# Kernel optimization log

Measured on AMD Instinct MI355X. Metric: run time of the kernel, lower is better.

## Reference

```python
import jax, jax.numpy as jnp
import numpy as np

B, S, D, E, K, FF = 4, 2048, 1024, 8, 2, 4096  # batch, seq, d_model, experts, top-k, 4*d_model


def setup_inputs() -> dict:
    key = jax.random.key(0)
    k0, k1, k2, k3 = jax.random.split(key, 4)
    scale = 0.02
    return {
        "x": jax.random.normal(k0, (B, S, D), jnp.float32),
        "gate_w": jax.random.normal(k1, (D, E), jnp.float32) * scale,
        "w1": jax.random.normal(k2, (E, D, FF), jnp.float32) * scale,
        "b1": jnp.zeros((E, FF), jnp.float32),
        "w2": jax.random.normal(k3, (E, FF, D), jnp.float32) * scale,
        "b2": jnp.zeros((E, D), jnp.float32),
    }


def reference(x, gate_w, w1, b1, w2, b2):
    # Gating: top-k logits, softmax over the selected k (matches torch.topk + softmax)
    logits = jnp.einsum("bsd,de->bse", x, gate_w)  # [B,S,E]
    vals, idxs = jax.lax.top_k(logits, K)           # [B,S,K]
    w = jax.nn.softmax(vals, axis=-1)               # [B,S,K]
    n_exp = gate_w.shape[-1]
    # Per-token combine weight for each expert (0 if not selected)
    combine = jnp.sum(jax.nn.one_hot(idxs, n_exp, dtype=x.dtype) * w[..., None], axis=-2)  # [B,S,E]

    out = jnp.zeros_like(x)
    for e in range(n_exp):  # fixed small loop over experts
        h = jax.nn.silu(jnp.einsum("bsd,df->bsf", x, w1[e]) + b1[e])  # dropout = identity (eval)
        y = jnp.einsum("bsf,fd->bsd", h, w2[e]) + b2[e]
        out = out + combine[..., e:e + 1] * y
    return out
```

## Files before the change

kernel.cpp:

```cpp
#include <hip/hip_runtime.h>
#include <math.h>

#define Tt 8192
#define Dd 1024
#define Ee 8
#define FFf 4096
#define SLOTS (Tt*2)

typedef unsigned short u16;
typedef unsigned int u32;
typedef __attribute__((ext_vector_type(8))) __bf16 bf16x8;
typedef __attribute__((ext_vector_type(4))) float f32x4;

__device__ __forceinline__ u16 f2bf(float f) {
  union { float f; u32 u; } v; v.f = f;
  u32 u = v.u;
  return (u16)((u + 0x7FFFu + ((u >> 16) & 1u)) >> 16);
}
__device__ __forceinline__ float bf2f(u16 h) {
  union { u32 u; float f; } v; v.u = ((u32)h) << 16; return v.f;
}
__device__ __forceinline__ void gl2lds16(const u16* g, u16* l) {
  __builtin_amdgcn_global_load_lds((const __attribute__((address_space(1))) void*)g,
                                   (__attribute__((address_space(3))) void*)l, 16, 0, 0);
}

__global__ void gate_topk_kernel(const float* __restrict__ x,
                                 const float* __restrict__ gw,
                                 int* __restrict__ counts,
                                 int* __restrict__ tok_e,
                                 float* __restrict__ tok_w) {
  int wave = (int)((blockIdx.x * blockDim.x + threadIdx.x) >> 6);
  int lane = threadIdx.x & 63;
  if (wave >= Tt) return;
  const float* xrow = x + (size_t)wave * Dd;
  float p[Ee];
#pragma unroll
  for (int e = 0; e < Ee; e++) p[e] = 0.f;
  int d0 = lane * 16;
#pragma unroll
  for (int i = 0; i < 16; i++) {
    float xv = xrow[d0 + i];
    const float* g = gw + (size_t)(d0 + i) * Ee;
#pragma unroll
    for (int e = 0; e < Ee; e++) p[e] += xv * g[e];
  }
#pragma unroll
  for (int e = 0; e < Ee; e++) {
    for (int off = 32; off > 0; off >>= 1) p[e] += __shfl_xor(p[e], off, 64);
  }
  if (lane == 0) {
    int e0 = 0; float v0 = p[0];
#pragma unroll
    for (int e = 1; e < Ee; e++) if (p[e] > v0) { v0 = p[e]; e0 = e; }
    int e1 = -1; float v1 = -INFINITY;
#pragma unroll
    for (int e = 0; e < Ee; e++) if (e != e0 && p[e] > v1) { v1 = p[e]; e1 = e; }
    float w0 = 1.f / (1.f + expf(v1 - v0));
    float w1 = 1.f - w0;
    tok_e[wave * 2 + 0] = e0; tok_e[wave * 2 + 1] = e1;
    tok_w[wave * 2 + 0] = w0; tok_w[wave * 2 + 1] = w1;
    atomicAdd(&counts[e0], 1);
    atomicAdd(&counts[e1], 1);
  }
}

__global__ void xb_convert_kernel(const float* __restrict__ x, u16* __restrict__ xb) {
  int i = blockIdx.x * blockDim.x + threadIdx.x;
  const float* s = x + (size_t)i * 8;
  f32x4 v0 = *(const f32x4*)(s);
  f32x4 v1 = *(const f32x4*)(s + 4);
  uint4 o;
  o.x = (u32)f2bf(v0[0]) | ((u32)f2bf(v0[1]) << 16);
  o.y = (u32)f2bf(v0[2]) | ((u32)f2bf(v0[3]) << 16);
  o.z = (u32)f2bf(v1[0]) | ((u32)f2bf(v1[1]) << 16);
  o.w = (u32)f2bf(v1[2]) | ((u32)f2bf(v1[3]) << 16);
  *(uint4*)(xb + (size_t)i * 8) = o;
}

__global__ __launch_bounds__(256) void wconv_kernel(const float* __restrict__ src,
                                                    u16* __restrict__ dst, int R, int C) {
  __shared__ float t[64][65];
  int e = blockIdx.z;
  size_t ebase = (size_t)e * R * C;
  int r0 = blockIdx.y * 64, c0 = blockIdx.x * 64;
  int tid = threadIdx.x;
  int row = tid >> 2, q = tid & 3;
  const float* sp = src + ebase + (size_t)(r0 + row) * C + c0 + q * 16;
  f32x4 v0 = *(const f32x4*)(sp);
  f32x4 v1 = *(const f32x4*)(sp + 4);
  f32x4 v2 = *(const f32x4*)(sp + 8);
  f32x4 v3 = *(const f32x4*)(sp + 12);
#pragma unroll
  for (int k = 0; k < 4; k++) t[row][q * 16 + k] = v0[k];
#pragma unroll
  for (int k = 0; k < 4; k++) t[row][q * 16 + 4 + k] = v1[k];
#pragma unroll
  for (int k = 0; k < 4; k++) t[row][q * 16 + 8 + k] = v2[k];
#pragma unroll
  for (int k = 0; k < 4; k++) t[row][q * 16 + 12 + k] = v3[k];
  __syncthreads();
  float c[16];
#pragma unroll
  for (int k = 0; k < 16; k++) c[k] = t[q * 16 + k][row];
  uint4 d0, d1;
  d0.x = (u32)f2bf(c[0]) | ((u32)f2bf(c[1]) << 16);
  d0.y = (u32)f2bf(c[2]) | ((u32)f2bf(c[3]) << 16);
  d0.z = (u32)f2bf(c[4]) | ((u32)f2bf(c[5]) << 16);
  d0.w = (u32)f2bf(c[6]) | ((u32)f2bf(c[7]) << 16);
  d1.x = (u32)f2bf(c[8]) | ((u32)f2bf(c[9]) << 16);
  d1.y = (u32)f2bf(c[10]) | ((u32)f2bf(c[11]) << 16);
  d1.z = (u32)f2bf(c[12]) | ((u32)f2bf(c[13]) << 16);
  d1.w = (u32)f2bf(c[14]) | ((u32)f2bf(c[15]) << 16);
  u16* dp = dst + ebase + (size_t)(c0 + row) * R + r0 + q * 16;
  *(uint4*)dp = d0;
  *(uint4*)(dp + 8) = d1;
}

__global__ void scan_kernel(const int* __restrict__ counts,
                            int* __restrict__ offsets, int* __restrict__ cursors) {
  if (threadIdx.x == 0 && blockIdx.x == 0) {
    int acc = 0;
    for (int e = 0; e < Ee; e++) { offsets[e] = acc; cursors[e] = acc; acc += counts[e]; }
  }
}

__global__ void scatter_kernel(const int* __restrict__ tok_e, const float* __restrict__ tok_w,
                               int* __restrict__ cursors,
                               int* __restrict__ slot_token, float* __restrict__ slot_w,
                               int* __restrict__ tok_slot) {
  int t = blockIdx.x * blockDim.x + threadIdx.x;
  if (t >= Tt) return;
#pragma unroll
  for (int k = 0; k < 2; k++) {
    int e = tok_e[t * 2 + k];
    int pos = atomicAdd(&cursors[e], 1);
    slot_token[pos] = t;
    slot_w[pos] = tok_w[t * 2 + k];
    tok_slot[t * 2 + k] = pos;
  }
}

#define MFMA16(H)                                                                 \
  do {                                                                            \
    acc[H][0][0] = __builtin_amdgcn_mfma_f32_16x16x32_bf16(a0, b0, acc[H][0][0], 0, 0, 0); \
    acc[H][0][1] = __builtin_amdgcn_mfma_f32_16x16x32_bf16(a0, b1, acc[H][0][1], 0, 0, 0); \
    acc[H][0][2] = __builtin_amdgcn_mfma_f32_16x16x32_bf16(a0, b2, acc[H][0][2], 0, 0, 0); \
    acc[H][0][3] = __builtin_amdgcn_mfma_f32_16x16x32_bf16(a0, b3, acc[H][0][3], 0, 0, 0); \
    acc[H][1][0] = __builtin_amdgcn_mfma_f32_16x16x32_bf16(a1, b0, acc[H][1][0], 0, 0, 0); \
    acc[H][1][1] = __builtin_amdgcn_mfma_f32_16x16x32_bf16(a1, b1, acc[H][1][1], 0, 0, 0); \
    acc[H][1][2] = __builtin_amdgcn_mfma_f32_16x16x32_bf16(a1, b2, acc[H][1][2], 0, 0, 0); \
    acc[H][1][3] = __builtin_amdgcn_mfma_f32_16x16x32_bf16(a1, b3, acc[H][1][3], 0, 0, 0); \
    acc[H][2][0] = __builtin_amdgcn_mfma_f32_16x16x32_bf16(a2, b0, acc[H][2][0], 0, 0, 0); \
    acc[H][2][1] = __builtin_amdgcn_mfma_f32_16x16x32_bf16(a2, b1, acc[H][2][1], 0, 0, 0); \
    acc[H][2][2] = __builtin_amdgcn_mfma_f32_16x16x32_bf16(a2, b2, acc[H][2][2], 0, 0, 0); \
    acc[H][2][3] = __builtin_amdgcn_mfma_f32_16x16x32_bf16(a2, b3, acc[H][2][3], 0, 0, 0); \
    acc[H][3][0] = __builtin_amdgcn_mfma_f32_16x16x32_bf16(a3, b0, acc[H][3][0], 0, 0, 0); \
    acc[H][3][1] = __builtin_amdgcn_mfma_f32_16x16x32_bf16(a3, b1, acc[H][3][1], 0, 0, 0); \
    acc[H][3][2] = __builtin_amdgcn_mfma_f32_16x16x32_bf16(a3, b2, acc[H][3][2], 0, 0, 0); \
    acc[H][3][3] = __builtin_amdgcn_mfma_f32_16x16x32_bf16(a3, b3, acc[H][3][3], 0, 0, 0); \
  } while (0)

template<int KDIM, int NDIM, int EPI, int GATHER>
__global__ __launch_bounds__(512, 2) void moe_gemm_big(
    const u16* __restrict__ A, const u16* __restrict__ BT,
    const float* __restrict__ bias,
    const int* __restrict__ offsets, const int* __restrict__ counts,
    const int* __restrict__ slot_token, const float* __restrict__ slot_w,
    u16* __restrict__ O16, float* __restrict__ Of) {
  constexpr int NT = KDIM / 64;
  int e = blockIdx.z;
  int cnt = counts[e];
  int rb = blockIdx.y;
  if (rb * 256 >= cnt) return;
  int off = offsets[e];
  int n0 = blockIdx.x * 256;

  __shared__ u16 S[65536];

  int tid = threadIdx.x;
  int lane = tid & 63, wave = tid >> 6;
  int wr = wave >> 2, wc = wave & 3;
  int lr = lane & 15, g = lane >> 4;

  const u16* BTe = BT + (size_t)e * NDIM * KDIM;

  const u16* aSrc[2][2];
  const u16* bSrc[2][2];
  int amax = off + cnt - 1;
#pragma unroll
  for (int h = 0; h < 2; h++)
#pragma unroll
    for (int s = 0; s < 2; s++) {
      int c = tid + s * 512;
      int lc = c ^ (((c >> 5) & 1) << 1);
      int ks = lc >> 9, rl = (lc >> 2) & 127, seg = lc & 3;
      int slotRow = off + rb * 256 + h * 128 + rl;
      if (slotRow > amax) slotRow = amax;
      int arow = GATHER ? slot_token[slotRow] : slotRow;
      aSrc[h][s] = A + (size_t)arow * KDIM + ks * 32 + seg * 8;
    }
#pragma unroll
  for (int ks = 0; ks < 2; ks++)
#pragma unroll
    for (int s = 0; s < 2; s++) {
      int c = tid + s * 512;
      int lc = c ^ (((c >> 5) & 1) << 1);
      int row = lc >> 2, seg = lc & 3;
      bSrc[ks][s] = BTe + (size_t)(n0 + row) * KDIM + ks * 32 + seg * 8;
    }

  auto stA = [&](int u, int h) {
    u16* d = &S[(u & 1) * 16384 + h * 8192 + wave * 512];
    gl2lds16(aSrc[h][0] + (size_t)u * 64, d);
    gl2lds16(aSrc[h][1] + (size_t)u * 64, d + 4096);
  };
  auto stB = [&](int u, int ks) {
    u16* d = &S[32768 + (u & 1) * 16384 + ks * 8192 + wave * 512];
    gl2lds16(bSrc[ks][0] + (size_t)u * 64, d);
    gl2lds16(bSrc[ks][1] + (size_t)u * 64, d + 4096);
  };
  auto rdA = [&](int dbuf, int hm, int ks, int i) -> bf16x8 {
    int rl = wr * 64 + i * 16 + lr;
    int logb = ks * 8192 + rl * 64 + g * 16;
    int phys = logb ^ (((rl >> 3) & 1) << 5);
    return *reinterpret_cast<const bf16x8*>(&S[dbuf * 16384 + hm * 8192 + (phys >> 1)]);
  };
  auto rdB = [&](int dbuf, int ks, int j) -> bf16x8 {
    int row = wc * 64 + j * 16 + lr;
    int logb = row * 64 + g * 16;
    int phys = logb ^ (((row >> 3) & 1) << 5);
    return *reinterpret_cast<const bf16x8*>(&S[32768 + dbuf * 16384 + ks * 8192 + (phys >> 1)]);
  };

  f32x4 acc[2][4][4];
#pragma unroll
  for (int h = 0; h < 2; h++)
#pragma unroll
    for (int i = 0; i < 4; i++)
#pragma unroll
      for (int j = 0; j < 4; j++) acc[h][i][j] = (f32x4)(0.0f);

  stB(0, 0); stA(0, 0); stA(0, 1); stB(0, 1);
  stB(1, 0); stA(1, 0);
  asm volatile("s_waitcnt vmcnt(4)" ::: "memory");
  __builtin_amdgcn_s_barrier();

  bf16x8 b0, b1, b2, b3;
  for (int t = 0; t < NT; ++t) {
    int dbuf = t & 1;
    {
      bf16x8 a0 = rdA(dbuf, 0, 0, 0), a1 = rdA(dbuf, 0, 0, 1),
             a2 = rdA(dbuf, 0, 0, 2), a3 = rdA(dbuf, 0, 0, 3);
      b0 = rdB(dbuf, 0, 0); b1 = rdB(dbuf, 0, 1); b2 = rdB(dbuf, 0, 2); b3 = rdB(dbuf, 0, 3);
      if (t + 1 < NT) stA(t + 1, 1);
      __builtin_amdgcn_s_barrier();
      asm volatile("s_waitcnt lgkmcnt(0)" ::: "memory");
      __builtin_amdgcn_sched_barrier(0);
      __builtin_amdgcn_s_setprio(1);
      MFMA16(0);
      __builtin_amdgcn_s_setprio(0);
      __builtin_amdgcn_s_barrier();
    }
    {
      bf16x8 a0 = rdA(dbuf, 1, 0, 0), a1 = rdA(dbuf, 1, 0, 1),
             a2 = rdA(dbuf, 1, 0, 2), a3 = rdA(dbuf, 1, 0, 3);
      if (t + 1 < NT) {
        stB(t + 1, 1);
        asm volatile("s_waitcnt vmcnt(6)" ::: "memory");
      }
      __builtin_amdgcn_s_barrier();
      asm volatile("s_waitcnt lgkmcnt(0)" ::: "memory");
      __builtin_amdgcn_sched_barrier(0);
      __builtin_amdgcn_s_setprio(1);
      MFMA16(1);
      __builtin_amdgcn_s_setprio(0);
      __builtin_amdgcn_s_barrier();
    }
    {
      bf16x8 a0 = rdA(dbuf, 0, 1, 0), a1 = rdA(dbuf, 0, 1, 1),
             a2 = rdA(dbuf, 0, 1, 2), a3 = rdA(dbuf, 0, 1, 3);
      b0 = rdB(dbuf, 1, 0); b1 = rdB(dbuf, 1, 1); b2 = rdB(dbuf, 1, 2); b3 = rdB(dbuf, 1, 3);
      if (t + 2 < NT) stB(t + 2, 0);
      __builtin_amdgcn_s_barrier();
      asm volatile("s_waitcnt lgkmcnt(0)" ::: "memory");
      __builtin_amdgcn_sched_barrier(0);
      __builtin_amdgcn_s_setprio(1);
      MFMA16(0);
      __builtin_amdgcn_s_setprio(0);
      __builtin_amdgcn_s_barrier();
    }
    {
      bf16x8 a0 = rdA(dbuf, 1, 1, 0), a1 = rdA(dbuf, 1, 1, 1),
             a2 = rdA(dbuf, 1, 1, 2), a3 = rdA(dbuf, 1, 1, 3);
      if (t + 2 < NT) {
        stA(t + 2, 0);
        asm volatile("s_waitcnt vmcnt(6)" ::: "memory");
      } else if (t + 1 < NT) {
        asm volatile("s_waitcnt vmcnt(0)" ::: "memory");
      }
      __builtin_amdgcn_s_barrier();
      asm volatile("s_waitcnt lgkmcnt(0)" ::: "memory");
      __builtin_amdgcn_sched_barrier(0);
      __builtin_amdgcn_s_setprio(1);
      MFMA16(1);
      __builtin_amdgcn_s_setprio(0);
      __builtin_amdgcn_s_barrier();
    }
  }

  int rlim = cnt - rb * 256;
#pragma unroll
  for (int hm = 0; hm < 2; hm++)
#pragma unroll
    for (int i = 0; i < 4; i++)
#pragma unroll
      for (int q = 0; q < 4; q++) {
        int m = hm * 128 + wr * 64 + i * 16 + g * 4 + q;
        if (m < rlim) {
          int slot = off + rb * 256 + m;
#pragma unroll
          for (int j = 0; j < 4; j++) {
            int n = n0 + wc * 64 + j * 16 + lr;
            float v = acc[hm][i][j][q] + bias[e * NDIM + n];
            if (EPI == 0) {
              float sv = v / (1.f + expf(-v));
              O16[(size_t)slot * NDIM + n] = f2bf(sv);
            } else if (EPI == 1) {
              O16[(size_t)slot * NDIM + n] = f2bf(v * slot_w[slot]);
            } else {
              atomicAdd(Of + (size_t)slot_token[slot] * NDIM + n, v * slot_w[slot]);
            }
          }
        }
      }
}

__global__ void combine_kernel(const u16* __restrict__ y, const int* __restrict__ tok_slot,
                               float* __restrict__ out) {
  int gid = blockIdx.x * blockDim.x + threadIdx.x;
  int t = gid >> 7;
  int seg = gid & 127;
  int s0 = tok_slot[t * 2 + 0], s1 = tok_slot[t * 2 + 1];
  uint4 a = *(const uint4*)(y + (size_t)s0 * Dd + seg * 8);
  uint4 b = *(const uint4*)(y + (size_t)s1 * Dd + seg * 8);
  f32x4 o0, o1;
  o0[0] = bf2f((u16)a.x) + bf2f((u16)b.x);
  o0[1] = bf2f((u16)(a.x >> 16)) + bf2f((u16)(b.x >> 16));
  o0[2] = bf2f((u16)a.y) + bf2f((u16)b.y);
  o0[3] = bf2f((u16)(a.y >> 16)) + bf2f((u16)(b.y >> 16));
  o1[0] = bf2f((u16)a.z) + bf2f((u16)b.z);
  o1[1] = bf2f((u16)(a.z >> 16)) + bf2f((u16)(b.z >> 16));
  o1[2] = bf2f((u16)a.w) + bf2f((u16)b.w);
  o1[3] = bf2f((u16)(a.w >> 16)) + bf2f((u16)(b.w >> 16));
  float* op = out + (size_t)t * Dd + seg * 8;
  *(f32x4*)op = o0;
  *(f32x4*)(op + 4) = o1;
}

extern "C" void kernel_launch(void* const* d_in, const int* in_sizes, int n_in,
                              void* d_out, int out_size, void* d_ws, size_t ws_size,
                              hipStream_t stream) {
  const float* x  = (const float*)d_in[0];
  const float* gw = (const float*)d_in[1];
  const float* w1 = (const float*)d_in[2];
  const float* b1 = (const float*)d_in[3];
  const float* w2 = (const float*)d_in[4];
  const float* b2 = (const float*)d_in[5];
  float* out = (float*)d_out;

  char* ws = (char*)d_ws;
  size_t off_counts = 0;
  size_t off_offsets = 256;
  size_t off_cursors = 512;
  size_t off_tok_e = 1024;
  size_t off_tok_w     = off_tok_e + (size_t)Tt * 2 * 4;
  size_t off_tok_slot  = off_tok_w + (size_t)Tt * 2 * 4;
  size_t off_slot_token= off_tok_slot + (size_t)Tt * 2 * 4;
  size_t off_slot_w    = off_slot_token + (size_t)SLOTS * 4;
  size_t off_xb        = off_slot_w + (size_t)SLOTS * 4;
  size_t off_h         = off_xb + (size_t)Tt * Dd * 2;
  size_t off_wT        = off_h + (size_t)SLOTS * FFf * 2;
  size_t off_y         = off_wT + (size_t)Ee * Dd * FFf * 2;
  size_t need_atomic   = off_y;
  size_t need_full     = off_y + (size_t)SLOTS * Dd * 2;
  if (ws_size < need_atomic) return;
  int use_combine = (ws_size >= need_full) ? 1 : 0;

  int* counts     = (int*)(ws + off_counts);
  int* offsets    = (int*)(ws + off_offsets);
  int* cursors    = (int*)(ws + off_cursors);
  int* tok_e      = (int*)(ws + off_tok_e);
  float* tok_w    = (float*)(ws + off_tok_w);
  int* tok_slot   = (int*)(ws + off_tok_slot);
  int* slot_token = (int*)(ws + off_slot_token);
  float* slot_w   = (float*)(ws + off_slot_w);
  u16* xb         = (u16*)(ws + off_xb);
  u16* h          = (u16*)(ws + off_h);
  u16* wT         = (u16*)(ws + off_wT);
  u16* y          = (u16*)(ws + off_y);

  hipMemsetAsync(ws, 0, 1024, stream);

  gate_topk_kernel<<<Tt / 4, 256, 0, stream>>>(x, gw, counts, tok_e, tok_w);
  xb_convert_kernel<<<(Tt * Dd / 8) / 256, 256, 0, stream>>>(x, xb);
  scan_kernel<<<1, 64, 0, stream>>>(counts, offsets, cursors);
  scatter_kernel<<<Tt / 256, 256, 0, stream>>>(tok_e, tok_w, cursors, slot_token, slot_w, tok_slot);

  {
    dim3 gc(FFf / 64, Dd / 64, Ee);
    wconv_kernel<<<gc, 256, 0, stream>>>(w1, wT, Dd, FFf);
  }
  {
    dim3 g1(FFf / 256, Tt / 256, Ee);
    moe_gemm_big<Dd, FFf, 0, 1><<<g1, 512, 0, stream>>>(xb, wT, b1, offsets, counts,
                                                        slot_token, slot_w, h, nullptr);
  }
  {
    dim3 gc(Dd / 64, FFf / 64, Ee);
    wconv_kernel<<<gc, 256, 0, stream>>>(w2, wT, FFf, Dd);
  }
  if (use_combine) {
    dim3 g2(Dd / 256, Tt / 256, Ee);
    moe_gemm_big<FFf, Dd, 1, 0><<<g2, 512, 0, stream>>>(h, wT, b2, offsets, counts,
                                                        slot_token, slot_w, y, nullptr);
    combine_kernel<<<(Tt * 128) / 256, 256, 0, stream>>>(y, tok_slot, out);
  } else {
    hipMemsetAsync(d_out, 0, (size_t)out_size * sizeof(float), stream);
    dim3 g2(Dd / 256, Tt / 256, Ee);
    moe_gemm_big<FFf, Dd, 2, 0><<<g2, 512, 0, stream>>>(h, wT, b2, offsets, counts,
                                                        slot_token, slot_w, nullptr, out);
  }
}
```

Baseline: 793.2 us.

## Shrink MoE GEMM row tile to 128 and fuse bf16 cast into gating

The grouped expert GEMM now uses a 128x256 output tile instead of 256x256. The k-step pipeline drops from four MFMA phases to two, shared memory shrinks, and the grid gets more blocks in the row dimension. This is meant to cut padding waste from ragged per-expert token counts and to spread work across more CUs, at the cost of less B-tile reuse per block. Separately, the fp32-to-bf16 conversion of x moves into the gating kernel, which already reads x, so the standalone conversion kernel and its extra pass over x are removed.

```diff
diff --git a/kernel.cpp b/kernel.cpp
--- a/kernel.cpp
+++ b/kernel.cpp
@@ -29,7 +29,8 @@
                                  const float* __restrict__ gw,
                                  int* __restrict__ counts,
                                  int* __restrict__ tok_e,
-                                 float* __restrict__ tok_w) {
+                                 float* __restrict__ tok_w,
+                                 u16* __restrict__ xb) {
   int wave = (int)((blockIdx.x * blockDim.x + threadIdx.x) >> 6);
   int lane = threadIdx.x & 63;
   if (wave >= Tt) return;
@@ -38,12 +39,27 @@
 #pragma unroll
   for (int e = 0; e < Ee; e++) p[e] = 0.f;
   int d0 = lane * 16;
+  float xv[16];
 #pragma unroll
   for (int i = 0; i < 16; i++) {
-    float xv = xrow[d0 + i];
+    xv[i] = xrow[d0 + i];
     const float* g = gw + (size_t)(d0 + i) * Ee;
 #pragma unroll
-    for (int e = 0; e < Ee; e++) p[e] += xv * g[e];
+    for (int e = 0; e < Ee; e++) p[e] += xv[i] * g[e];
+  }
+  {
+    uint4 o0, o1;
+    o0.x = (u32)f2bf(xv[0]) | ((u32)f2bf(xv[1]) << 16);
+    o0.y = (u32)f2bf(xv[2]) | ((u32)f2bf(xv[3]) << 16);
+    o0.z = (u32)f2bf(xv[4]) | ((u32)f2bf(xv[5]) << 16);
+    o0.w = (u32)f2bf(xv[6]) | ((u32)f2bf(xv[7]) << 16);
+    o1.x = (u32)f2bf(xv[8]) | ((u32)f2bf(xv[9]) << 16);
+    o1.y = (u32)f2bf(xv[10]) | ((u32)f2bf(xv[11]) << 16);
+    o1.z = (u32)f2bf(xv[12]) | ((u32)f2bf(xv[13]) << 16);
+    o1.w = (u32)f2bf(xv[14]) | ((u32)f2bf(xv[15]) << 16);
+    u16* dp = xb + (size_t)wave * Dd + d0;
+    *(uint4*)dp = o0;
+    *(uint4*)(dp + 8) = o1;
   }
 #pragma unroll
   for (int e = 0; e < Ee; e++) {
@@ -63,19 +79,6 @@
     atomicAdd(&counts[e0], 1);
     atomicAdd(&counts[e1], 1);
   }
-}
-
-__global__ void xb_convert_kernel(const float* __restrict__ x, u16* __restrict__ xb) {
-  int i = blockIdx.x * blockDim.x + threadIdx.x;
-  const float* s = x + (size_t)i * 8;
-  f32x4 v0 = *(const f32x4*)(s);
-  f32x4 v1 = *(const f32x4*)(s + 4);
-  uint4 o;
-  o.x = (u32)f2bf(v0[0]) | ((u32)f2bf(v0[1]) << 16);
-  o.y = (u32)f2bf(v0[2]) | ((u32)f2bf(v0[3]) << 16);
-  o.z = (u32)f2bf(v1[0]) | ((u32)f2bf(v1[1]) << 16);
-  o.w = (u32)f2bf(v1[2]) | ((u32)f2bf(v1[3]) << 16);
-  *(uint4*)(xb + (size_t)i * 8) = o;
 }
 
 __global__ __launch_bounds__(256) void wconv_kernel(const float* __restrict__ src,
@@ -141,28 +144,28 @@
   }
 }
 
-#define MFMA16(H)                                                                 \
+#define MFMA16R                                                                   \
   do {                                                                            \
-    acc[H][0][0] = __builtin_amdgcn_mfma_f32_16x16x32_bf16(a0, b0, acc[H][0][0], 0, 0, 0); \
-    acc[H][0][1] = __builtin_amdgcn_mfma_f32_16x16x32_bf16(a0, b1, acc[H][0][1], 0, 0, 0); \
-    acc[H][0][2] = __builtin_amdgcn_mfma_f32_16x16x32_bf16(a0, b2, acc[H][0][2], 0, 0, 0); \
-    acc[H][0][3] = __builtin_amdgcn_mfma_f32_16x16x32_bf16(a0, b3, acc[H][0][3], 0, 0, 0); \
-    acc[H][1][0] = __builtin_amdgcn_mfma_f32_16x16x32_bf16(a1, b0, acc[H][1][0], 0, 0, 0); \
-    acc[H][1][1] = __builtin_amdgcn_mfma_f32_16x16x32_bf16(a1, b1, acc[H][1][1], 0, 0, 0); \
-    acc[H][1][2] = __builtin_amdgcn_mfma_f32_16x16x32_bf16(a1, b2, acc[H][1][2], 0, 0, 0); \
-    acc[H][1][3] = __builtin_amdgcn_mfma_f32_16x16x32_bf16(a1, b3, acc[H][1][3], 0, 0, 0); \
-    acc[H][2][0] = __builtin_amdgcn_mfma_f32_16x16x32_bf16(a2, b0, acc[H][2][0], 0, 0, 0); \
-    acc[H][2][1] = __builtin_amdgcn_mfma_f32_16x16x32_bf16(a2, b1, acc[H][2][1], 0, 0, 0); \
-    acc[H][2][2] = __builtin_amdgcn_mfma_f32_16x16x32_bf16(a2, b2, acc[H][2][2], 0, 0, 0); \
-    acc[H][2][3] = __builtin_amdgcn_mfma_f32_16x16x32_bf16(a2, b3, acc[H][2][3], 0, 0, 0); \
-    acc[H][3][0] = __builtin_amdgcn_mfma_f32_16x16x32_bf16(a3, b0, acc[H][3][0], 0, 0, 0); \
-    acc[H][3][1] = __builtin_amdgcn_mfma_f32_16x16x32_bf16(a3, b1, acc[H][3][1], 0, 0, 0); \
-    acc[H][3][2] = __builtin_amdgcn_mfma_f32_16x16x32_bf16(a3, b2, acc[H][3][2], 0, 0, 0); \
-    acc[H][3][3] = __builtin_amdgcn_mfma_f32_16x16x32_bf16(a3, b3, acc[H][3][3], 0, 0, 0); \
+    acc[0][0] = __builtin_amdgcn_mfma_f32_16x16x32_bf16(a0, b0, acc[0][0], 0, 0, 0); \
+    acc[0][1] = __builtin_amdgcn_mfma_f32_16x16x32_bf16(a0, b1, acc[0][1], 0, 0, 0); \
+    acc[0][2] = __builtin_amdgcn_mfma_f32_16x16x32_bf16(a0, b2, acc[0][2], 0, 0, 0); \
+    acc[0][3] = __builtin_amdgcn_mfma_f32_16x16x32_bf16(a0, b3, acc[0][3], 0, 0, 0); \
+    acc[1][0] = __builtin_amdgcn_mfma_f32_16x16x32_bf16(a1, b0, acc[1][0], 0, 0, 0); \
+    acc[1][1] = __builtin_amdgcn_mfma_f32_16x16x32_bf16(a1, b1, acc[1][1], 0, 0, 0); \
+    acc[1][2] = __builtin_amdgcn_mfma_f32_16x16x32_bf16(a1, b2, acc[1][2], 0, 0, 0); \
+    acc[1][3] = __builtin_amdgcn_mfma_f32_16x16x32_bf16(a1, b3, acc[1][3], 0, 0, 0); \
+    acc[2][0] = __builtin_amdgcn_mfma_f32_16x16x32_bf16(a2, b0, acc[2][0], 0, 0, 0); \
+    acc[2][1] = __builtin_amdgcn_mfma_f32_16x16x32_bf16(a2, b1, acc[2][1], 0, 0, 0); \
+    acc[2][2] = __builtin_amdgcn_mfma_f32_16x16x32_bf16(a2, b2, acc[2][2], 0, 0, 0); \
+    acc[2][3] = __builtin_amdgcn_mfma_f32_16x16x32_bf16(a2, b3, acc[2][3], 0, 0, 0); \
+    acc[3][0] = __builtin_amdgcn_mfma_f32_16x16x32_bf16(a3, b0, acc[3][0], 0, 0, 0); \
+    acc[3][1] = __builtin_amdgcn_mfma_f32_16x16x32_bf16(a3, b1, acc[3][1], 0, 0, 0); \
+    acc[3][2] = __builtin_amdgcn_mfma_f32_16x16x32_bf16(a3, b2, acc[3][2], 0, 0, 0); \
+    acc[3][3] = __builtin_amdgcn_mfma_f32_16x16x32_bf16(a3, b3, acc[3][3], 0, 0, 0); \
   } while (0)
 
 template<int KDIM, int NDIM, int EPI, int GATHER>
-__global__ __launch_bounds__(512, 2) void moe_gemm_big(
+__global__ __launch_bounds__(512, 2) void moe_gemm_r(
     const u16* __restrict__ A, const u16* __restrict__ BT,
     const float* __restrict__ bias,
     const int* __restrict__ offsets, const int* __restrict__ counts,
@@ -172,11 +175,11 @@
   int e = blockIdx.z;
   int cnt = counts[e];
   int rb = blockIdx.y;
-  if (rb * 256 >= cnt) return;
+  if (rb * 128 >= cnt) return;
   int off = offsets[e];
   int n0 = blockIdx.x * 256;
 
-  __shared__ u16 S[65536];
+  __shared__ u16 S[49152];
 
   int tid = threadIdx.x;
   int lane = tid & 63, wave = tid >> 6;
@@ -185,117 +188,85 @@
 
   const u16* BTe = BT + (size_t)e * NDIM * KDIM;
 
-  const u16* aSrc[2][2];
-  const u16* bSrc[2][2];
+  const u16* aSrc[2];
+  const u16* bSrc[4];
   int amax = off + cnt - 1;
 #pragma unroll
-  for (int h = 0; h < 2; h++)
-#pragma unroll
-    for (int s = 0; s < 2; s++) {
-      int c = tid + s * 512;
-      int lc = c ^ (((c >> 5) & 1) << 1);
-      int ks = lc >> 9, rl = (lc >> 2) & 127, seg = lc & 3;
-      int slotRow = off + rb * 256 + h * 128 + rl;
-      if (slotRow > amax) slotRow = amax;
-      int arow = GATHER ? slot_token[slotRow] : slotRow;
-      aSrc[h][s] = A + (size_t)arow * KDIM + ks * 32 + seg * 8;
-    }
-#pragma unroll
-  for (int ks = 0; ks < 2; ks++)
-#pragma unroll
-    for (int s = 0; s < 2; s++) {
-      int c = tid + s * 512;
-      int lc = c ^ (((c >> 5) & 1) << 1);
-      int row = lc >> 2, seg = lc & 3;
-      bSrc[ks][s] = BTe + (size_t)(n0 + row) * KDIM + ks * 32 + seg * 8;
-    }
-
-  auto stA = [&](int u, int h) {
-    u16* d = &S[(u & 1) * 16384 + h * 8192 + wave * 512];
-    gl2lds16(aSrc[h][0] + (size_t)u * 64, d);
-    gl2lds16(aSrc[h][1] + (size_t)u * 64, d + 4096);
+  for (int s = 0; s < 2; s++) {
+    int c = tid + s * 512;
+    int lc = c ^ (((c >> 5) & 1) << 1);
+    int rl = (lc >> 2) & 127, seg = lc & 3;
+    int slotRow = off + rb * 128 + rl;
+    if (slotRow > amax) slotRow = amax;
+    int arow = GATHER ? slot_token[slotRow] : slotRow;
+    aSrc[s] = A + (size_t)arow * KDIM + s * 32 + seg * 8;
+  }
+#pragma unroll
+  for (int s = 0; s < 4; s++) {
+    int c = tid + s * 512;
+    int lc = c ^ (((c >> 5) & 1) << 1);
+    int row = (lc >> 2) & 255, seg = lc & 3;
+    int ks = s >> 1;
+    bSrc[s] = BTe + (size_t)(n0 + row) * KDIM + ks * 32 + seg * 8;
+  }
+
+  auto stA = [&](int u, int ks) {
+    gl2lds16(aSrc[ks] + (size_t)u * 64, &S[(u & 1) * 8192 + ks * 4096 + wave * 512]);
   };
   auto stB = [&](int u, int ks) {
-    u16* d = &S[32768 + (u & 1) * 16384 + ks * 8192 + wave * 512];
-    gl2lds16(bSrc[ks][0] + (size_t)u * 64, d);
-    gl2lds16(bSrc[ks][1] + (size_t)u * 64, d + 4096);
+    u16* base = &S[16384 + (u & 1) * 16384 + ks * 8192 + wave * 512];
+    gl2lds16(bSrc[ks * 2] + (size_t)u * 64, base);
+    gl2lds16(bSrc[ks * 2 + 1] + (size_t)u * 64, base + 4096);
   };
-  auto rdA = [&](int dbuf, int hm, int ks, int i) -> bf16x8 {
+  auto rdA = [&](int dbuf, int ks, int i) -> bf16x8 {
     int rl = wr * 64 + i * 16 + lr;
-    int logb = ks * 8192 + rl * 64 + g * 16;
+    int logb = rl * 64 + g * 16;
     int phys = logb ^ (((rl >> 3) & 1) << 5);
-    return *reinterpret_cast<const bf16x8*>(&S[dbuf * 16384 + hm * 8192 + (phys >> 1)]);
+    return *reinterpret_cast<const bf16x8*>(&S[dbuf * 8192 + ks * 4096 + (phys >> 1)]);
   };
   auto rdB = [&](int dbuf, int ks, int j) -> bf16x8 {
     int row = wc * 64 + j * 16 + lr;
     int logb = row * 64 + g * 16;
     int phys = logb ^ (((row >> 3) & 1) << 5);
-    return *reinterpret_cast<const bf16x8*>(&S[32768 + dbuf * 16384 + ks * 8192 + (phys >> 1)]);
+    return *reinterpret_cast<const bf16x8*>(&S[16384 + dbuf * 16384 + ks * 8192 + (phys >> 1)]);
   };
 
-  f32x4 acc[2][4][4];
-#pragma unroll
-  for (int h = 0; h < 2; h++)
-#pragma unroll
-    for (int i = 0; i < 4; i++)
-#pragma unroll
-      for (int j = 0; j < 4; j++) acc[h][i][j] = (f32x4)(0.0f);
-
-  stB(0, 0); stA(0, 0); stA(0, 1); stB(0, 1);
+  f32x4 acc[4][4];
+#pragma unroll
+  for (int i = 0; i < 4; i++)
+#pragma unroll
+    for (int j = 0; j < 4; j++) acc[i][j] = (f32x4)(0.0f);
+
+  stB(0, 0); stA(0, 0);
+  stB(0, 1); stA(0, 1);
   stB(1, 0); stA(1, 0);
-  asm volatile("s_waitcnt vmcnt(4)" ::: "memory");
+  asm volatile("s_waitcnt vmcnt(3)" ::: "memory");
   __builtin_amdgcn_s_barrier();
 
-  bf16x8 b0, b1, b2, b3;
   for (int t = 0; t < NT; ++t) {
     int dbuf = t & 1;
     {
-      bf16x8 a0 = rdA(dbuf, 0, 0, 0), a1 = rdA(dbuf, 0, 0, 1),
-             a2 = rdA(dbuf, 0, 0, 2), a3 = rdA(dbuf, 0, 0, 3);
-      b0 = rdB(dbuf, 0, 0); b1 = rdB(dbuf, 0, 1); b2 = rdB(dbuf, 0, 2); b3 = rdB(dbuf, 0, 3);
-      if (t + 1 < NT) stA(t + 1, 1);
+      bf16x8 a0 = rdA(dbuf, 0, 0), a1 = rdA(dbuf, 0, 1),
+             a2 = rdA(dbuf, 0, 2), a3 = rdA(dbuf, 0, 3);
+      bf16x8 b0 = rdB(dbuf, 0, 0), b1 = rdB(dbuf, 0, 1),
+             b2 = rdB(dbuf, 0, 2), b3 = rdB(dbuf, 0, 3);
+      if (t + 1 < NT) { stB(t + 1, 1); stA(t + 1, 1); }
       __builtin_amdgcn_s_barrier();
       asm volatile("s_waitcnt lgkmcnt(0)" ::: "memory");
       __builtin_amdgcn_sched_barrier(0);
       __builtin_amdgcn_s_setprio(1);
-      MFMA16(0);
+      MFMA16R;
       __builtin_amdgcn_s_setprio(0);
       __builtin_amdgcn_s_barrier();
     }
     {
-      bf16x8 a0 = rdA(dbuf, 1, 0, 0), a1 = rdA(dbuf, 1, 0, 1),
-             a2 = rdA(dbuf, 1, 0, 2), a3 = rdA(dbuf, 1, 0, 3);
-      if (t + 1 < NT) {
-        stB(t + 1, 1);
-        asm volatile("s_waitcnt vmcnt(6)" ::: "memory");
-      }
-      __builtin_amdgcn_s_barrier();
-      asm volatile("s_waitcnt lgkmcnt(0)" ::: "memory");
-      __builtin_amdgcn_sched_barrier(0);
-      __builtin_amdgcn_s_setprio(1);
-      MFMA16(1);
-      __builtin_amdgcn_s_setprio(0);
-      __builtin_amdgcn_s_barrier();
-    }
-    {
-      bf16x8 a0 = rdA(dbuf, 0, 1, 0), a1 = rdA(dbuf, 0, 1, 1),
-             a2 = rdA(dbuf, 0, 1, 2), a3 = rdA(dbuf, 0, 1, 3);
-      b0 = rdB(dbuf, 1, 0); b1 = rdB(dbuf, 1, 1); b2 = rdB(dbuf, 1, 2); b3 = rdB(dbuf, 1, 3);
-      if (t + 2 < NT) stB(t + 2, 0);
-      __builtin_amdgcn_s_barrier();
-      asm volatile("s_waitcnt lgkmcnt(0)" ::: "memory");
-      __builtin_amdgcn_sched_barrier(0);
-      __builtin_amdgcn_s_setprio(1);
-      MFMA16(0);
-      __builtin_amdgcn_s_setprio(0);
-      __builtin_amdgcn_s_barrier();
-    }
-    {
-      bf16x8 a0 = rdA(dbuf, 1, 1, 0), a1 = rdA(dbuf, 1, 1, 1),
-             a2 = rdA(dbuf, 1, 1, 2), a3 = rdA(dbuf, 1, 1, 3);
+      bf16x8 a0 = rdA(dbuf, 1, 0), a1 = rdA(dbuf, 1, 1),
+             a2 = rdA(dbuf, 1, 2), a3 = rdA(dbuf, 1, 3);
+      bf16x8 b0 = rdB(dbuf, 1, 0), b1 = rdB(dbuf, 1, 1),
+             b2 = rdB(dbuf, 1, 2), b3 = rdB(dbuf, 1, 3);
       if (t + 2 < NT) {
-        stA(t + 2, 0);
-        asm volatile("s_waitcnt vmcnt(6)" ::: "memory");
+        stB(t + 2, 0); stA(t + 2, 0);
+        asm volatile("s_waitcnt vmcnt(3)" ::: "memory");
       } else if (t + 1 < NT) {
         asm volatile("s_waitcnt vmcnt(0)" ::: "memory");
       }
@@ -303,37 +274,35 @@
       asm volatile("s_waitcnt lgkmcnt(0)" ::: "memory");
       __builtin_amdgcn_sched_barrier(0);
       __builtin_amdgcn_s_setprio(1);
-      MFMA16(1);
+      MFMA16R;
       __builtin_amdgcn_s_setprio(0);
       __builtin_amdgcn_s_barrier();
     }
   }
 
-  int rlim = cnt - rb * 256;
-#pragma unroll
-  for (int hm = 0; hm < 2; hm++)
-#pragma unroll
-    for (int i = 0; i < 4; i++)
-#pragma unroll
-      for (int q = 0; q < 4; q++) {
-        int m = hm * 128 + wr * 64 + i * 16 + g * 4 + q;
-        if (m < rlim) {
-          int slot = off + rb * 256 + m;
-#pragma unroll
-          for (int j = 0; j < 4; j++) {
-            int n = n0 + wc * 64 + j * 16 + lr;
-            float v = acc[hm][i][j][q] + bias[e * NDIM + n];
-            if (EPI == 0) {
-              float sv = v / (1.f + expf(-v));
-              O16[(size_t)slot * NDIM + n] = f2bf(sv);
-            } else if (EPI == 1) {
-              O16[(size_t)slot * NDIM + n] = f2bf(v * slot_w[slot]);
-            } else {
-              atomicAdd(Of + (size_t)slot_token[slot] * NDIM + n, v * slot_w[slot]);
-            }
+  int rlim = cnt - rb * 128;
+#pragma unroll
+  for (int i = 0; i < 4; i++)
+#pragma unroll
+    for (int q = 0; q < 4; q++) {
+      int m = wr * 64 + i * 16 + g * 4 + q;
+      if (m < rlim) {
+        int slot = off + rb * 128 + m;
+#pragma unroll
+        for (int j = 0; j < 4; j++) {
+          int n = n0 + wc * 64 + j * 16 + lr;
+          float v = acc[i][j][q] + bias[e * NDIM + n];
+          if (EPI == 0) {
+            float sv = v / (1.f + expf(-v));
+            O16[(size_t)slot * NDIM + n] = f2bf(sv);
+          } else if (EPI == 1) {
+            O16[(size_t)slot * NDIM + n] = f2bf(v * slot_w[slot]);
+          } else {
+            atomicAdd(Of + (size_t)slot_token[slot] * NDIM + n, v * slot_w[slot]);
           }
         }
       }
+    }
 }
 
 __global__ void combine_kernel(const u16* __restrict__ y, const int* __restrict__ tok_slot,
@@ -402,8 +371,7 @@
 
   hipMemsetAsync(ws, 0, 1024, stream);
 
-  gate_topk_kernel<<<Tt / 4, 256, 0, stream>>>(x, gw, counts, tok_e, tok_w);
-  xb_convert_kernel<<<(Tt * Dd / 8) / 256, 256, 0, stream>>>(x, xb);
+  gate_topk_kernel<<<Tt / 4, 256, 0, stream>>>(x, gw, counts, tok_e, tok_w, xb);
   scan_kernel<<<1, 64, 0, stream>>>(counts, offsets, cursors);
   scatter_kernel<<<Tt / 256, 256, 0, stream>>>(tok_e, tok_w, cursors, slot_token, slot_w, tok_slot);
 
@@ -412,23 +380,23 @@
     wconv_kernel<<<gc, 256, 0, stream>>>(w1, wT, Dd, FFf);
   }
   {
-    dim3 g1(FFf / 256, Tt / 256, Ee);
-    moe_gemm_big<Dd, FFf, 0, 1><<<g1, 512, 0, stream>>>(xb, wT, b1, offsets, counts,
-                                                        slot_token, slot_w, h, nullptr);
+    dim3 g1(FFf / 256, 64, Ee);
+    moe_gemm_r<Dd, FFf, 0, 1><<<g1, 512, 0, stream>>>(xb, wT, b1, offsets, counts,
+                                                      slot_token, slot_w, h, nullptr);
   }
   {
     dim3 gc(Dd / 64, FFf / 64, Ee);
     wconv_kernel<<<gc, 256, 0, stream>>>(w2, wT, FFf, Dd);
   }
   if (use_combine) {
-    dim3 g2(Dd / 256, Tt / 256, Ee);
-    moe_gemm_big<FFf, Dd, 1, 0><<<g2, 512, 0, stream>>>(h, wT, b2, offsets, counts,
-                                                        slot_token, slot_w, y, nullptr);
+    dim3 g2(Dd / 256, 64, Ee);
+    moe_gemm_r<FFf, Dd, 1, 0><<<g2, 512, 0, stream>>>(h, wT, b2, offsets, counts,
+                                                      slot_token, slot_w, y, nullptr);
     combine_kernel<<<(Tt * 128) / 256, 256, 0, stream>>>(y, tok_slot, out);
   } else {
     hipMemsetAsync(d_out, 0, (size_t)out_size * sizeof(float), stream);
-    dim3 g2(Dd / 256, Tt / 256, Ee);
-    moe_gemm_big<FFf, Dd, 2, 0><<<g2, 512, 0, stream>>>(h, wT, b2, offsets, counts,
-                                                        slot_token, slot_w, nullptr, out);
-  }
-}
+    dim3 g2(Dd / 256, 64, Ee);
+    moe_gemm_r<FFf, Dd, 2, 0><<<g2, 512, 0, stream>>>(h, wT, b2, offsets, counts,
+                                                      slot_token, slot_w, nullptr, out);
+  }
+}
```

Result: slower. 823.2 us (+3.8%).
